# Kernel optimization log

Measured on AMD Instinct MI355X. Metric: run time of the kernel, lower is better.

## Reference

```python
import jax, jax.numpy as jnp
from jax import lax
import numpy as np

BATCH, T, N, S = 512, 1024, 64, 32


def setup_inputs() -> dict:
    key = jax.random.key(0)
    k1, k2, k3, k4 = jax.random.split(key, 4)
    return {
        "inputs": jax.random.uniform(k1, (BATCH, T, S), dtype=jnp.float32),
        "emission_kernel": jax.random.normal(k2, (N, S), dtype=jnp.float32),
        "transition_kernel": jax.random.normal(k3, (N, N), dtype=jnp.float32),
        "init_kernel": jax.random.normal(k4, (N,), dtype=jnp.float32),
    }


def reference(inputs, emission_kernel, transition_kernel, init_kernel):
    # HMM forward algorithm with per-step normalization (scaled forward vars).
    A = jax.nn.softmax(transition_kernel, axis=-1)   # [n, n] transition
    B = jax.nn.softmax(emission_kernel, axis=-1)     # [n, s] emission
    I = jax.nn.softmax(init_kernel, axis=-1)         # [n]   initial dist

    batch, n = inputs.shape[0], A.shape[0]
    # Emission likelihoods for all timesteps at once (same math as per-step matvec)
    E_all = jnp.einsum('ns,bts->tbn', B, inputs)     # [T, batch, n]

    def step(carry, e_t):
        is_init, fwd, loglik = carry
        # R = is_init * I  +  A^T @ fwd   (matvec(A, fwd, transpose_a=True))
        R = is_init[:, None] * I[None, :] + fwd @ A          # [batch, n]
        f = e_t * R                                          # [batch, n]
        Ssum = jnp.sum(f, axis=-1)                           # [batch]
        loglik = loglik + jnp.log(Ssum)
        f = f / Ssum[:, None]
        return (jnp.zeros_like(is_init), f, loglik), (f, loglik)

    init = (jnp.ones((batch,), dtype=jnp.float32),
            jnp.zeros((batch, n), dtype=jnp.float32),
            jnp.zeros((batch,), dtype=jnp.float32))
    _, (fwds, lls) = lax.scan(step, init, E_all)
    fwds = jnp.swapaxes(fwds, 0, 1)                  # [batch, T, n]
    lls = jnp.swapaxes(lls, 0, 1)                    # [batch, T]
    # Pack (forward vars, running loglik) into one array: [batch, T, n+1]
    return jnp.concatenate([fwds, lls[..., None]], axis=-1)
```

## Files before the change

### kernel.cpp

```cpp
#include <hip/hip_runtime.h>

#define BATCH 512
#define TT    1024
#define NST   64
#define NSYM  32
#define NCH   64
#define CLEN  16
#define WARM  12
#define LN2F  0.69314718055994530942f

#define AP_MV    6400
#define AP_EM    8448
#define WS_STATS 9472

typedef _Float16 f16x8 __attribute__((ext_vector_type(8)));
typedef float    f32x4 __attribute__((ext_vector_type(4)));

#define MFMA_F16(a,b,c) __builtin_amdgcn_mfma_f32_16x16x32_f16(a,b,c,0,0,0)

__device__ __forceinline__ unsigned pkrtz_u(float a, float b) {
    return __builtin_bit_cast(unsigned, __builtin_amdgcn_cvt_pkrtz(a, b));
}

__device__ __forceinline__ int sigma_k(int g, int r) {
    return (r < 4) ? (4 * g + r) : (16 + 4 * g + (r - 4));
}

__device__ __forceinline__ f16x8 pk8(float a0, float a1, float a2, float a3,
                                     float a4, float a5, float a6, float a7) {
    union U { unsigned u[4]; f16x8 v; } u;
    u.u[0] = pkrtz_u(a0, a1);
    u.u[1] = pkrtz_u(a2, a3);
    u.u[2] = pkrtz_u(a4, a5);
    u.u[3] = pkrtz_u(a6, a7);
    return u.v;
}

__global__ __launch_bounds__(64) void hmm_prep(
    const float* __restrict__ em, const float* __restrict__ tr,
    const float* __restrict__ ini, float* __restrict__ ws)
{
    const int n = threadIdx.x;

    {
        float a[64];
        float m = -1e30f;
        #pragma unroll
        for (int j = 0; j < 64; ++j) { a[j] = tr[n * 64 + j]; m = fmaxf(m, a[j]); }
        float s = 0.f;
        #pragma unroll
        for (int j = 0; j < 64; ++j) { a[j] = __expf(a[j] - m); s += a[j]; }
        const float inv = 1.f / s;
        #pragma unroll
        for (int j = 0; j < 64; ++j) ws[n * 64 + j] = a[j] * inv;
    }
    {
        float bv[32];
        float m = -1e30f;
        #pragma unroll
        for (int j = 0; j < 32; ++j) { bv[j] = em[n * 32 + j]; m = fmaxf(m, bv[j]); }
        float s = 0.f;
        #pragma unroll
        for (int j = 0; j < 32; ++j) { bv[j] = __expf(bv[j] - m); s += bv[j]; }
        const float inv = 1.f / s;
        #pragma unroll
        for (int j = 0; j < 32; ++j) ws[4096 + n * 32 + j] = bv[j] * inv;
    }
    {
        float v = ini[n];
        float m = v;
        #pragma unroll
        for (int off = 32; off; off >>= 1) m = fmaxf(m, __shfl_xor(m, off, 64));
        const float e = __expf(v - m);
        float s = e;
        #pragma unroll
        for (int off = 32; off; off >>= 1) s += __shfl_xor(s, off, 64);
        ws[6144 + n] = e / s;
    }

    __syncthreads();

    const int g   = n >> 4;
    const int cl  = n & 15;
    unsigned* wsu = (unsigned*)ws;

    #pragma unroll
    for (int mt = 0; mt < 4; ++mt) {
        #pragma unroll
        for (int kc = 0; kc < 2; ++kc) {
            #pragma unroll
            for (int p = 0; p < 4; ++p) {
                const int k0 = sigma_k(g, 2 * p);
                const int k1 = sigma_k(g, 2 * p + 1);
                const int m  = 16 * mt + cl;
                const float a0 = ws[(32 * kc + k0) * 64 + m];
                const float a1 = ws[(32 * kc + k1) * 64 + m];
                wsu[AP_MV + ((mt * 2 + kc) * 64 + n) * 4 + p] = pkrtz_u(a0, a1);
            }
        }
        #pragma unroll
        for (int p = 0; p < 4; ++p) {
            const int k0 = sigma_k(g, 2 * p);
            const int k1 = sigma_k(g, 2 * p + 1);
            const int st = 16 * mt + cl;
            const float b0 = ws[4096 + st * 32 + k0];
            const float b1 = ws[4096 + st * 32 + k1];
            wsu[AP_EM + (mt * 64 + n) * 4 + p] = pkrtz_u(b0, b1);
        }
    }
}

__global__ __launch_bounds__(64, 1) void hmm_scan(
    const float* __restrict__ inputs, float* __restrict__ ws,
    float* __restrict__ out)
{
    const int lane = threadIdx.x;
    const int col  = lane & 15;
    const int g    = lane >> 4;
    const int b    = blockIdx.x >> 2;
    const int w    = blockIdx.x & 3;
    const int c    = 16 * w + col;
    const int t0   = c * CLEN;
    const bool isc0 = (c == 0);

    __shared__ int4 fl[12][64];
    f16x8 Amv[4][2], Aem[4];
    {
        const int4* mvp = (const int4*)((const unsigned*)ws + AP_MV);
        const int4* emp = (const int4*)((const unsigned*)ws + AP_EM);
        #pragma unroll
        for (int j = 0; j < 8; ++j) fl[j][lane] = mvp[j * 64 + lane];
        #pragma unroll
        for (int j = 0; j < 4; ++j) fl[8 + j][lane] = emp[j * 64 + lane];
        __syncthreads();
        #pragma unroll
        for (int mt = 0; mt < 4; ++mt) {
            Amv[mt][0] = __builtin_bit_cast(f16x8, fl[mt * 2 + 0][lane]);
            Amv[mt][1] = __builtin_bit_cast(f16x8, fl[mt * 2 + 1][lane]);
            Aem[mt]    = __builtin_bit_cast(f16x8, fl[8 + mt][lane]);
        }
        #pragma unroll
        for (int mt = 0; mt < 4; ++mt)
            asm volatile("" : "+v"(Amv[mt][0]), "+v"(Amv[mt][1]), "+v"(Aem[mt]));
    }

    const float* __restrict__ xp = inputs + (size_t)b * (TT * NSYM);
    float* __restrict__ op       = out    + (size_t)b * (TT * 65);

    float4 rga[4], rgb[4];
    auto loadx = [&](int k, int s) {
        int t = t0 + k;
        t = t < 0 ? 0 : t;
        t = t > TT - 1 ? TT - 1 : t;
        const float* row = xp + (size_t)t * NSYM;
        rga[s] = *(const float4*)(row + 4 * g);
        rgb[s] = *(const float4*)(row + 16 + 4 * g);
    };

    float hD[4][4];
    #pragma unroll
    for (int mt = 0; mt < 4; ++mt)
        #pragma unroll
        for (int r = 0; r < 4; ++r) hD[mt][r] = 1.0f;
    int Esum = 0;

    const f32x4 z4 = {0.f, 0.f, 0.f, 0.f};

    auto step = [&](int k, int s, bool store_) {
        if (store_) {
            float p = 0.f;
            #pragma unroll
            for (int mt = 0; mt < 4; ++mt)
                #pragma unroll
                for (int r = 0; r < 4; ++r) p += hD[mt][r];
            p += __shfl_xor(p, 16, 64);
            p += __shfl_xor(p, 32, 64);
            const float rS = __builtin_amdgcn_rcpf(p);
            float* rowp = op + (size_t)(t0 + k - 1) * 65;
            #pragma unroll
            for (int mt = 0; mt < 4; ++mt) {
                const float4 v4 = {hD[mt][0] * rS, hD[mt][1] * rS,
                                   hD[mt][2] * rS, hD[mt][3] * rS};
                *(float4*)(rowp + 16 * mt + 4 * g) = v4;
            }
            if (g == 0) rowp[64] = __logf(p) + (float)Esum * LN2F;
        }
        const int pb = __builtin_amdgcn_readlane(__float_as_int(hD[0][0]), 15);
        int ex = (pb >> 23) & 255;
        ex = ex < 1 ? 1 : (ex > 253 ? 253 : ex);
        const float sc = __uint_as_float((unsigned)(254 - ex) << 23);
        Esum += ex - 127;
        const f16x8 bx = pk8(rga[s].x, rga[s].y, rga[s].z, rga[s].w,
                             rgb[s].x, rgb[s].y, rgb[s].z, rgb[s].w);
        f32x4 Esc[4];
        #pragma unroll
        for (int mt = 0; mt < 4; ++mt) {
            const f32x4 E = MFMA_F16(Aem[mt], bx, z4);
            Esc[mt][0] = E[0] * sc; Esc[mt][1] = E[1] * sc;
            Esc[mt][2] = E[2] * sc; Esc[mt][3] = E[3] * sc;
        }
        const f16x8 bh0 = pk8(hD[0][0], hD[0][1], hD[0][2], hD[0][3],
                              hD[1][0], hD[1][1], hD[1][2], hD[1][3]);
        const f16x8 bh1 = pk8(hD[2][0], hD[2][1], hD[2][2], hD[2][3],
                              hD[3][0], hD[3][1], hD[3][2], hD[3][3]);
        f32x4 mva[4], mvb[4];
        #pragma unroll
        for (int mt = 0; mt < 4; ++mt) {
            mva[mt] = MFMA_F16(Amv[mt][0], bh0, z4);
            mvb[mt] = MFMA_F16(Amv[mt][1], bh1, z4);
        }
        #pragma unroll
        for (int mt = 0; mt < 4; ++mt)
            #pragma unroll
            for (int r = 0; r < 4; ++r)
                hD[mt][r] = Esc[mt][r] * (mva[mt][r] + mvb[mt][r]);
        loadx(k + 4, s);
    };

    #pragma unroll
    for (int s = 0; s < 4; ++s) loadx(-WARM + s, s);

    for (int kk = -WARM; kk < 0; kk += 4) {
        #pragma unroll
        for (int s = 0; s < 4; ++s) step(kk + s, s, false);
    }

    float Lstart;
    {
        float p = 0.f;
        #pragma unroll
        for (int mt = 0; mt < 4; ++mt)
            #pragma unroll
            for (int r = 0; r < 4; ++r) p += hD[mt][r];
        p += __shfl_xor(p, 16, 64);
        p += __shfl_xor(p, 32, 64);
        Lstart = __logf(p) + (float)Esum * LN2F;
    }
    Lstart = isc0 ? 0.f : Lstart;

    step(0, 0, false);

    {
        const float* row = xp;
        const float4 xa = *(const float4*)(row + 4 * g);
        const float4 xb = *(const float4*)(row + 16 + 4 * g);
        const f16x8 bx0 = pk8(xa.x, xa.y, xa.z, xa.w, xb.x, xb.y, xb.z, xb.w);
        #pragma unroll
        for (int mt = 0; mt < 4; ++mt) {
            const f32x4 E0 = MFMA_F16(Aem[mt], bx0, z4);
            const float4 iv = *(const float4*)(ws + 6144 + 16 * mt + 4 * g);
            const float ivv[4] = {iv.x, iv.y, iv.z, iv.w};
            #pragma unroll
            for (int r = 0; r < 4; ++r)
                if (isc0) hD[mt][r] = E0[r] * ivv[r];
        }
        if (isc0) Esum = 0;
    }

    #pragma unroll
    for (int s = 1; s < 4; ++s) step(s, s, true);
    #pragma unroll
    for (int kk = 4; kk <= 12; kk += 4) {
        #pragma unroll
        for (int s = 0; s < 4; ++s) step(kk + s, s, true);
    }

    {
        float p = 0.f;
        #pragma unroll
        for (int mt = 0; mt < 4; ++mt)
            #pragma unroll
            for (int r = 0; r < 4; ++r) p += hD[mt][r];
        p += __shfl_xor(p, 16, 64);
        p += __shfl_xor(p, 32, 64);
        const float rS = __builtin_amdgcn_rcpf(p);
        float* rowp = op + (size_t)(t0 + CLEN - 1) * 65;
        #pragma unroll
        for (int mt = 0; mt < 4; ++mt) {
            const float4 v4 = {hD[mt][0] * rS, hD[mt][1] * rS,
                               hD[mt][2] * rS, hD[mt][3] * rS};
            *(float4*)(rowp + 16 * mt + 4 * g) = v4;
        }
        if (g == 0) {
            rowp[64] = __logf(p) + (float)Esum * LN2F;
            ws[WS_STATS + (size_t)b * NCH + c] = Lstart;
        }
    }
}

__global__ __launch_bounds__(64) void hmm_fix(
    const float* __restrict__ ws, float* __restrict__ out)
{
    const int b    = blockIdx.x;
    const int lane = threadIdx.x;

    float* __restrict__ op = out + (size_t)b * (TT * 65);

    const float Ls = ws[WS_STATS + (size_t)b * NCH + lane];
    const float Le = op[(size_t)(lane * CLEN + CLEN - 1) * 65 + 64];
    const float D  = Le - Ls;

    float O = 0.f;
    #pragma unroll
    for (int j = 0; j < NCH - 1; ++j) {
        const float Dj = __int_as_float(
            __builtin_amdgcn_readlane(__float_as_int(D), j));
        if (lane > j) O += Dj;
    }
    const float offs = O - Ls;

    #pragma unroll
    for (int k = 0; k < 16; ++k) {
        const int row  = k * 64 + lane;
        const int cidx = row >> 4;
        const float offk = __shfl(offs, cidx, 64);
        op[(size_t)row * 65 + 64] += offk;
    }
}

extern "C" void kernel_launch(void* const* d_in, const int* in_sizes, int n_in,
                              void* d_out, int out_size, void* d_ws, size_t ws_size,
                              hipStream_t stream) {
    const float* inputs = (const float*)d_in[0];
    const float* em     = (const float*)d_in[1];
    const float* tr     = (const float*)d_in[2];
    const float* ini    = (const float*)d_in[3];
    float* out = (float*)d_out;
    float* ws  = (float*)d_ws;

    hmm_prep<<<1, 64, 0, stream>>>(em, tr, ini, ws);
    hmm_scan<<<BATCH * 4, 64, 0, stream>>>(inputs, ws, out);
    hmm_fix<<<BATCH, 64, 0, stream>>>(ws, out);
}
```

Baseline: 70.07 us.

## Stage output rows in swizzled LDS and flush as contiguous float4 writes

Each step now writes its normalized forward variables and log-likelihood into a shared-memory buffer instead of issuing scattered, misaligned float4 stores straight to global memory. Every four steps the wave flushes each chunk's four rows (260 contiguous floats) with aligned, coalesced float4 stores, using an XOR swizzle to limit LDS bank conflicts. The weight fragments are also loaded directly from global memory rather than bounced through LDS with a barrier. The cost is extra LDS traffic, address arithmetic and a larger LDS footprint per block.

New measurement: 73.70 us. +5.2%, slower.

```diff
diff --git a/kernel.cpp b/kernel.cpp
--- a/kernel.cpp
+++ b/kernel.cpp
@@ -35,6 +35,8 @@
     u.u[3] = pkrtz_u(a6, a7);
     return u.v;
 }
+
+__device__ __forceinline__ int swz(int d) { return d ^ ((d >> 7) & 28); }
 
 __global__ __launch_bounds__(64) void hmm_prep(
     const float* __restrict__ em, const float* __restrict__ tr,
@@ -123,21 +125,17 @@
     const int t0   = c * CLEN;
     const bool isc0 = (c == 0);
 
-    __shared__ int4 fl[12][64];
+    __shared__ float obuf[16 * 4 * 65];
+
     f16x8 Amv[4][2], Aem[4];
     {
         const int4* mvp = (const int4*)((const unsigned*)ws + AP_MV);
         const int4* emp = (const int4*)((const unsigned*)ws + AP_EM);
         #pragma unroll
-        for (int j = 0; j < 8; ++j) fl[j][lane] = mvp[j * 64 + lane];
-        #pragma unroll
-        for (int j = 0; j < 4; ++j) fl[8 + j][lane] = emp[j * 64 + lane];
-        __syncthreads();
-        #pragma unroll
         for (int mt = 0; mt < 4; ++mt) {
-            Amv[mt][0] = __builtin_bit_cast(f16x8, fl[mt * 2 + 0][lane]);
-            Amv[mt][1] = __builtin_bit_cast(f16x8, fl[mt * 2 + 1][lane]);
-            Aem[mt]    = __builtin_bit_cast(f16x8, fl[8 + mt][lane]);
+            Amv[mt][0] = __builtin_bit_cast(f16x8, mvp[(mt * 2 + 0) * 64 + lane]);
+            Amv[mt][1] = __builtin_bit_cast(f16x8, mvp[(mt * 2 + 1) * 64 + lane]);
+            Aem[mt]    = __builtin_bit_cast(f16x8, emp[mt * 64 + lane]);
         }
         #pragma unroll
         for (int mt = 0; mt < 4; ++mt)
@@ -166,6 +164,28 @@
 
     const f32x4 z4 = {0.f, 0.f, 0.f, 0.f};
 
+    auto flushW = [&](int kk0) {
+        #pragma unroll
+        for (int rnd = 0; rnd < 16; ++rnd) {
+            const int idx  = rnd * 64 + lane;
+            const int grp  = idx / 65;
+            const int dloc = (idx - grp * 65) * 4;
+            const int dden = grp * 260 + dloc;
+            const float4 v = *(const float4*)&obuf[swz(dden)];
+            *(float4*)(op + (size_t)(256 * w + 16 * grp + kk0) * 65 + dloc) = v;
+        }
+        {
+            if (lane < 16) {
+                const int idx  = 1024 + lane;
+                const int grp  = idx / 65;
+                const int dloc = (idx - grp * 65) * 4;
+                const int dden = grp * 260 + dloc;
+                const float4 v = *(const float4*)&obuf[swz(dden)];
+                *(float4*)(op + (size_t)(256 * w + 16 * grp + kk0) * 65 + dloc) = v;
+            }
+        }
+    };
+
     auto step = [&](int k, int s, bool store_) {
         if (store_) {
             float p = 0.f;
@@ -176,14 +196,13 @@
             p += __shfl_xor(p, 16, 64);
             p += __shfl_xor(p, 32, 64);
             const float rS = __builtin_amdgcn_rcpf(p);
-            float* rowp = op + (size_t)(t0 + k - 1) * 65;
-            #pragma unroll
-            for (int mt = 0; mt < 4; ++mt) {
-                const float4 v4 = {hD[mt][0] * rS, hD[mt][1] * rS,
-                                   hD[mt][2] * rS, hD[mt][3] * rS};
-                *(float4*)(rowp + 16 * mt + 4 * g) = v4;
-            }
-            if (g == 0) rowp[64] = __logf(p) + (float)Esum * LN2F;
+            const int db = col * 260 + ((k - 1) & 3) * 65;
+            #pragma unroll
+            for (int mt = 0; mt < 4; ++mt)
+                #pragma unroll
+                for (int r = 0; r < 4; ++r)
+                    obuf[swz(db + 16 * mt + 4 * g + r)] = hD[mt][r] * rS;
+            if (g == 0) obuf[swz(db + 64)] = __logf(p) + (float)Esum * LN2F;
         }
         const int pb = __builtin_amdgcn_readlane(__float_as_int(hD[0][0]), 15);
         int ex = (pb >> 23) & 255;
@@ -219,7 +238,6 @@
 
     #pragma unroll
     for (int s = 0; s < 4; ++s) loadx(-WARM + s, s);
-
     for (int kk = -WARM; kk < 0; kk += 4) {
         #pragma unroll
         for (int s = 0; s < 4; ++s) step(kk + s, s, false);
@@ -241,9 +259,8 @@
     step(0, 0, false);
 
     {
-        const float* row = xp;
-        const float4 xa = *(const float4*)(row + 4 * g);
-        const float4 xb = *(const float4*)(row + 16 + 4 * g);
+        const float4 xa = *(const float4*)(xp + 4 * g);
+        const float4 xb = *(const float4*)(xp + 16 + 4 * g);
         const f16x8 bx0 = pk8(xa.x, xa.y, xa.z, xa.w, xb.x, xb.y, xb.z, xb.w);
         #pragma unroll
         for (int mt = 0; mt < 4; ++mt) {
@@ -258,11 +275,11 @@
     }
 
     #pragma unroll
-    for (int s = 1; s < 4; ++s) step(s, s, true);
-    #pragma unroll
-    for (int kk = 4; kk <= 12; kk += 4) {
-        #pragma unroll
-        for (int s = 0; s < 4; ++s) step(kk + s, s, true);
+    for (int k = 1; k <= 15; ++k) {
+        step(k, k & 3, true);
+        if (k == 4)  flushW(0);
+        if (k == 8)  flushW(4);
+        if (k == 12) flushW(8);
     }
 
     {
@@ -274,18 +291,18 @@
         p += __shfl_xor(p, 16, 64);
         p += __shfl_xor(p, 32, 64);
         const float rS = __builtin_amdgcn_rcpf(p);
-        float* rowp = op + (size_t)(t0 + CLEN - 1) * 65;
-        #pragma unroll
-        for (int mt = 0; mt < 4; ++mt) {
-            const float4 v4 = {hD[mt][0] * rS, hD[mt][1] * rS,
-                               hD[mt][2] * rS, hD[mt][3] * rS};
-            *(float4*)(rowp + 16 * mt + 4 * g) = v4;
-        }
+        const int db = col * 260 + 3 * 65;
+        #pragma unroll
+        for (int mt = 0; mt < 4; ++mt)
+            #pragma unroll
+            for (int r = 0; r < 4; ++r)
+                obuf[swz(db + 16 * mt + 4 * g + r)] = hD[mt][r] * rS;
         if (g == 0) {
-            rowp[64] = __logf(p) + (float)Esum * LN2F;
+            obuf[swz(db + 64)] = __logf(p) + (float)Esum * LN2F;
             ws[WS_STATS + (size_t)b * NCH + c] = Lstart;
         }
     }
+    flushW(12);
 }
 
 __global__ __launch_bounds__(64) void hmm_fix(
```

## Stage chunk inputs as fp16 in LDS and shorten warmup

Applied to the files above, without the earlier changes.

Each block now cooperatively loads its chunk's input rows (plus warmup history) once, converts them to packed fp16 and stores them in a swizzled shared-memory buffer. Per-step reads then come from LDS instead of a global-load ring. Warmup drops from 12 to 8 steps, and the two matvec MFMAs now chain through the accumulator rather than being added afterwards. The A matrices are also read directly from global memory instead of through LDS. Fewer warmup steps cuts serial work but may reduce accuracy at chunk boundaries, and the upfront staging plus barrier adds latency before the scan starts.

Result: faster. 61.55 us, median of 2 (-12.2%).

```diff
diff --git a/kernel.cpp b/kernel.cpp
--- a/kernel.cpp
+++ b/kernel.cpp
@@ -6,7 +6,7 @@
 #define NSYM  32
 #define NCH   64
 #define CLEN  16
-#define WARM  12
+#define WARM  8
 #define LN2F  0.69314718055994530942f
 
 #define AP_MV    6400
@@ -35,6 +35,8 @@
     u.u[3] = pkrtz_u(a6, a7);
     return u.v;
 }
+
+__device__ __forceinline__ int swz16(int d) { return d ^ (((d >> 8) & 7) << 2); }
 
 __global__ __launch_bounds__(64) void hmm_prep(
     const float* __restrict__ em, const float* __restrict__ tr,
@@ -123,38 +125,50 @@
     const int t0   = c * CLEN;
     const bool isc0 = (c == 0);
 
-    __shared__ int4 fl[12][64];
+    __shared__ unsigned xs16[272 * 16];
+
     f16x8 Amv[4][2], Aem[4];
     {
         const int4* mvp = (const int4*)((const unsigned*)ws + AP_MV);
         const int4* emp = (const int4*)((const unsigned*)ws + AP_EM);
         #pragma unroll
-        for (int j = 0; j < 8; ++j) fl[j][lane] = mvp[j * 64 + lane];
-        #pragma unroll
-        for (int j = 0; j < 4; ++j) fl[8 + j][lane] = emp[j * 64 + lane];
-        __syncthreads();
-        #pragma unroll
-        for (int mt = 0; mt < 4; ++mt) {
-            Amv[mt][0] = __builtin_bit_cast(f16x8, fl[mt * 2 + 0][lane]);
-            Amv[mt][1] = __builtin_bit_cast(f16x8, fl[mt * 2 + 1][lane]);
-            Aem[mt]    = __builtin_bit_cast(f16x8, fl[8 + mt][lane]);
-        }
-        #pragma unroll
-        for (int mt = 0; mt < 4; ++mt)
-            asm volatile("" : "+v"(Amv[mt][0]), "+v"(Amv[mt][1]), "+v"(Aem[mt]));
+        for (int mt = 0; mt < 4; ++mt) {
+            Amv[mt][0] = __builtin_bit_cast(f16x8, mvp[(mt * 2 + 0) * 64 + lane]);
+            Amv[mt][1] = __builtin_bit_cast(f16x8, mvp[(mt * 2 + 1) * 64 + lane]);
+            Aem[mt]    = __builtin_bit_cast(f16x8, emp[mt * 64 + lane]);
+        }
     }
 
     const float* __restrict__ xp = inputs + (size_t)b * (TT * NSYM);
     float* __restrict__ op       = out    + (size_t)b * (TT * 65);
 
-    float4 rga[4], rgb[4];
-    auto loadx = [&](int k, int s) {
-        int t = t0 + k;
-        t = t < 0 ? 0 : t;
-        t = t > TT - 1 ? TT - 1 : t;
-        const float* row = xp + (size_t)t * NSYM;
-        rga[s] = *(const float4*)(row + 4 * g);
-        rgb[s] = *(const float4*)(row + 16 + 4 * g);
+    #pragma unroll
+    for (int i = 0; i < 17; ++i) {
+        const int d   = (i * 64 + lane) * 4;
+        const int row = d >> 4;
+        const int sy  = (d & 15) * 2;
+        int grow = 256 * w - 16 + row;
+        grow = grow < 0 ? 0 : grow;
+        const float* src = xp + (size_t)grow * 32 + sy;
+        const float4 a  = *(const float4*)(src);
+        const float4 bq = *(const float4*)(src + 4);
+        unsigned* pdst = &xs16[swz16(d)];
+        pdst[0] = pkrtz_u(a.x, a.y);
+        pdst[1] = pkrtz_u(a.z, a.w);
+        pdst[2] = pkrtz_u(bq.x, bq.y);
+        pdst[3] = pkrtz_u(bq.z, bq.w);
+    }
+    __syncthreads();
+
+    auto ldx = [&](int k) -> f16x8 {
+        const int row = col * 16 + k + 16;
+        const int d0  = row * 16 + 2 * g;
+        const int d1  = d0 + 8;
+        union { unsigned u[4]; f16x8 v; } r;
+        const uint2 lo = *(const uint2*)&xs16[swz16(d0)];
+        const uint2 hi = *(const uint2*)&xs16[swz16(d1)];
+        r.u[0] = lo.x; r.u[1] = lo.y; r.u[2] = hi.x; r.u[3] = hi.y;
+        return r.v;
     };
 
     float hD[4][4];
@@ -166,7 +180,7 @@
 
     const f32x4 z4 = {0.f, 0.f, 0.f, 0.f};
 
-    auto step = [&](int k, int s, bool store_) {
+    auto step = [&](int k, bool store_) {
         if (store_) {
             float p = 0.f;
             #pragma unroll
@@ -190,8 +204,7 @@
         ex = ex < 1 ? 1 : (ex > 253 ? 253 : ex);
         const float sc = __uint_as_float((unsigned)(254 - ex) << 23);
         Esum += ex - 127;
-        const f16x8 bx = pk8(rga[s].x, rga[s].y, rga[s].z, rga[s].w,
-                             rgb[s].x, rgb[s].y, rgb[s].z, rgb[s].w);
+        const f16x8 bx = ldx(k);
         f32x4 Esc[4];
         #pragma unroll
         for (int mt = 0; mt < 4; ++mt) {
@@ -203,27 +216,19 @@
                               hD[1][0], hD[1][1], hD[1][2], hD[1][3]);
         const f16x8 bh1 = pk8(hD[2][0], hD[2][1], hD[2][2], hD[2][3],
                               hD[3][0], hD[3][1], hD[3][2], hD[3][3]);
-        f32x4 mva[4], mvb[4];
-        #pragma unroll
-        for (int mt = 0; mt < 4; ++mt) {
-            mva[mt] = MFMA_F16(Amv[mt][0], bh0, z4);
-            mvb[mt] = MFMA_F16(Amv[mt][1], bh1, z4);
-        }
-        #pragma unroll
-        for (int mt = 0; mt < 4; ++mt)
-            #pragma unroll
-            for (int r = 0; r < 4; ++r)
-                hD[mt][r] = Esc[mt][r] * (mva[mt][r] + mvb[mt][r]);
-        loadx(k + 4, s);
+        #pragma unroll
+        for (int mt = 0; mt < 4; ++mt) {
+            const f32x4 mv = MFMA_F16(Amv[mt][1], bh1,
+                              MFMA_F16(Amv[mt][0], bh0, z4));
+            hD[mt][0] = Esc[mt][0] * mv[0];
+            hD[mt][1] = Esc[mt][1] * mv[1];
+            hD[mt][2] = Esc[mt][2] * mv[2];
+            hD[mt][3] = Esc[mt][3] * mv[3];
+        }
     };
 
-    #pragma unroll
-    for (int s = 0; s < 4; ++s) loadx(-WARM + s, s);
-
-    for (int kk = -WARM; kk < 0; kk += 4) {
-        #pragma unroll
-        for (int s = 0; s < 4; ++s) step(kk + s, s, false);
-    }
+    #pragma unroll 4
+    for (int k = -WARM; k < 0; ++k) step(k, false);
 
     float Lstart;
     {
@@ -238,13 +243,10 @@
     }
     Lstart = isc0 ? 0.f : Lstart;
 
-    step(0, 0, false);
-
-    {
-        const float* row = xp;
-        const float4 xa = *(const float4*)(row + 4 * g);
-        const float4 xb = *(const float4*)(row + 16 + 4 * g);
-        const f16x8 bx0 = pk8(xa.x, xa.y, xa.z, xa.w, xb.x, xb.y, xb.z, xb.w);
+    step(0, false);
+
+    {
+        const f16x8 bx0 = ldx(0);
         #pragma unroll
         for (int mt = 0; mt < 4; ++mt) {
             const f32x4 E0 = MFMA_F16(Aem[mt], bx0, z4);
@@ -258,12 +260,7 @@
     }
 
     #pragma unroll
-    for (int s = 1; s < 4; ++s) step(s, s, true);
-    #pragma unroll
-    for (int kk = 4; kk <= 12; kk += 4) {
-        #pragma unroll
-        for (int s = 0; s < 4; ++s) step(kk + s, s, true);
-    }
+    for (int k = 1; k <= 15; ++k) step(k, true);
 
     {
         float p = 0.f;
```
